# Optimization experiments

Measured on AMD Instinct MI355X. Metric: run time of the kernel, lower is better.

## Reference

```python
import jax, jax.numpy as jnp
import numpy as np

N = 4096      # nodes
F = 128       # input feature dim
HEADS = 8     # attention_num
U = 8         # units per head


def setup_inputs() -> dict:
    key = jax.random.key(0)
    k_a, k_h, k_w, k_al, k_ar = jax.random.split(key, 5)
    A = jax.random.randint(k_a, (N, N), 0, 2).astype(jnp.float32)   # dense 0/1 adjacency
    H = jax.random.normal(k_h, (N, F), dtype=jnp.float32)
    W = jax.random.normal(k_w, (HEADS, F, U), dtype=jnp.float32) * 0.1
    a_left = jax.random.normal(k_al, (HEADS, U), dtype=jnp.float32) * 0.1
    a_right = jax.random.normal(k_ar, (HEADS, U), dtype=jnp.float32) * 0.1
    return {"A": A, "H": H, "W": W, "a_left": a_left, "a_right": a_right}


def reference(A, H, W, a_left, a_right):
    # Per-head attention logits: E[h,i,j] = e_left[h,i] + e_right[h,j]
    e_l = jnp.einsum('nf,hfu,hu->hn', H, W, a_left)    # [HEADS, N]
    e_r = jnp.einsum('nf,hfu,hu->hn', H, W, a_right)   # [HEADS, N]
    E = e_l[:, :, None] + e_r[:, None, :]              # [HEADS, N, N]
    # Faithful to original: denominator uses exp(E * A) (zeros in A -> exp(0)=1)
    denom = jnp.sum(jnp.exp(E * A[None]), axis=-1, keepdims=True)   # [HEADS, N, 1]
    Alpha = jnp.exp(E) / denom * A[None]               # masked attention weights
    # Aggregate then project: elu(Alpha @ H @ W) per head
    out = jax.nn.elu(jnp.einsum('hij,jf,hfu->hiu', Alpha, H, W))    # [HEADS, N, U]
    # is_output_layer=False -> concat heads along feature dim: [N, HEADS*U]
    return jnp.transpose(out, (1, 0, 2)).reshape(H.shape[0], HEADS * U)
```

## Files before the change

kernel.cpp:

```cpp
#include <hip/hip_runtime.h>
#include <hip/hip_bf16.h>

#define NN 4096
#define FF 128
#define NC 80
#define HPAD 136

typedef __attribute__((ext_vector_type(4))) float float4v;
typedef __attribute__((ext_vector_type(4))) unsigned int uint4v;
typedef __attribute__((ext_vector_type(8))) short short8;
typedef __attribute__((ext_vector_type(8))) unsigned short ushort8;
typedef __attribute__((ext_vector_type(4))) unsigned short ushort4v;

static __device__ inline unsigned short bfb(float x) {
    __hip_bfloat16 b = __float2bfloat16(x);
    return *(unsigned short*)&b;
}
static __device__ inline float bff(unsigned short u) {
    __hip_bfloat16 b = *(__hip_bfloat16*)&u;
    return __bfloat162float(b);
}

__global__ __launch_bounds__(128) void gat_prep(const float* __restrict__ H,
                                                const float* __restrict__ W,
                                                const float* __restrict__ al,
                                                const float* __restrict__ ar,
                                                float* __restrict__ expEl,
                                                __hip_bfloat16* __restrict__ Bp)
{
    __shared__ unsigned short Hhi[32 * HPAD], Hlo[32 * HPAD];
    __shared__ unsigned short Whi[16 * NC * 8], Wlo[16 * NC * 8];
    const int t  = threadIdx.x;
    const int j0 = blockIdx.x * 32;

    {
        const int jr = t >> 2, f0 = (t & 3) * 32;
        const float* src = H + (size_t)(j0 + jr) * FF + f0;
        unsigned short* dh = Hhi + jr * HPAD + f0;
        unsigned short* dl = Hlo + jr * HPAD + f0;
        #pragma unroll
        for (int i = 0; i < 32; i += 4) {
            float4v x = *(const float4v*)(src + i);
            ushort4v hv, lv;
            #pragma unroll
            for (int c2 = 0; c2 < 4; ++c2) {
                unsigned short h = bfb(x[c2]);
                hv[c2] = h;
                lv[c2] = bfb(x[c2] - bff(h));
            }
            *(ushort4v*)(dh + i) = hv;
            *(ushort4v*)(dl + i) = lv;
        }
    }
    {
        const int hu = t & 63;
        const int fb = (t >> 6) * 64;
        const float* wsrc = W + (size_t)(hu >> 3) * (FF * 8) + (hu & 7);
        #pragma unroll
        for (int g8 = 0; g8 < 8; ++g8) {
            const int f0 = fb + g8 * 8;
            ushort8 hv, lv;
            #pragma unroll
            for (int i = 0; i < 8; ++i) {
                float x = wsrc[(size_t)(f0 + i) * 8];
                unsigned short h = bfb(x);
                hv[i] = h; lv[i] = bfb(x - bff(h));
            }
            const int g = (f0 >> 5) * 4 + ((f0 >> 3) & 3);
            *(ushort8*)&Whi[((size_t)g * NC + hu) * 8] = hv;
            *(ushort8*)&Wlo[((size_t)g * NC + hu) * 8] = lv;
        }
    }
    {
        const int h  = t >> 4;
        const int f0 = (t & 15) * 8;
        float arv[8], alv[8];
        #pragma unroll
        for (int u = 0; u < 8; ++u) { arv[u] = ar[h * 8 + u]; alv[u] = al[h * 8 + u]; }
        ushort8 rh, rl, lh, ll;
        #pragma unroll
        for (int i = 0; i < 8; ++i) {
            const float* wp = W + (size_t)h * (FF * 8) + (size_t)(f0 + i) * 8;
            float sr = 0.f, sl = 0.f;
            #pragma unroll
            for (int u = 0; u < 8; ++u) { float w = wp[u]; sr += w * arv[u]; sl += w * alv[u]; }
            unsigned short a = bfb(sr); rh[i] = a; rl[i] = bfb(sr - bff(a));
            unsigned short b = bfb(sl); lh[i] = b; ll[i] = bfb(sl - bff(b));
        }
        const int g = (f0 >> 5) * 4 + ((f0 >> 3) & 3);
        *(ushort8*)&Whi[((size_t)g * NC + 64 + h) * 8] = rh;
        *(ushort8*)&Wlo[((size_t)g * NC + 64 + h) * 8] = rl;
        *(ushort8*)&Whi[((size_t)g * NC + 72 + h) * 8] = lh;
        *(ushort8*)&Wlo[((size_t)g * NC + 72 + h) * 8] = ll;
    }
    __syncthreads();

    const int w = t >> 6, lane = t & 63;
    const int m16 = lane & 15, q = lane >> 4;

    float4v acc[5] = {};
    #pragma unroll
    for (int kt = 0; kt < 4; ++kt) {
        short8 ahi = *(const short8*)&Hhi[(w * 16 + m16) * HPAD + kt * 32 + q * 8];
        short8 alo = *(const short8*)&Hlo[(w * 16 + m16) * HPAD + kt * 32 + q * 8];
        #pragma unroll
        for (int nt = 0; nt < 5; ++nt) {
            short8 bhi = *(const short8*)&Whi[((size_t)(kt * 4 + q) * NC + nt * 16 + m16) * 8];
            short8 blo = *(const short8*)&Wlo[((size_t)(kt * 4 + q) * NC + nt * 16 + m16) * 8];
            acc[nt] = __builtin_amdgcn_mfma_f32_16x16x32_bf16(ahi, bhi, acc[nt], 0, 0, 0);
            acc[nt] = __builtin_amdgcn_mfma_f32_16x16x32_bf16(alo, bhi, acc[nt], 0, 0, 0);
            acc[nt] = __builtin_amdgcn_mfma_f32_16x16x32_bf16(ahi, blo, acc[nt], 0, 0, 0);
        }
    }

    const int jbase = j0 + w * 16 + q * 4;
    float ex[4];
    #pragma unroll
    for (int r = 0; r < 4; ++r) ex[r] = expf(acc[4][r]);
    if (m16 >= 8) {
        #pragma unroll
        for (int r = 0; r < 4; ++r)
            expEl[(m16 - 8) * NN + jbase + r] = ex[r];
    }
    #pragma unroll
    for (int r = 0; r < 4; ++r) {
        const int j = jbase + r;
        const size_t base = ((size_t)((j >> 5) * 4 + ((j >> 3) & 3)) * NC) * 8 + (j & 7);
        #pragma unroll
        for (int nt = 0; nt < 4; ++nt) {
            const int srcl = (lane & 48) | (nt * 2 + (m16 >> 3));
            const float er = __shfl(ex[r], srcl);
            Bp[base + (size_t)(nt * 16 + m16) * 8] = __float2bfloat16(er * acc[nt][r]);
        }
        const float v = (m16 < 8) ? ex[r] : (m16 == 8 ? 1.0f : 0.0f);
        Bp[base + (size_t)(64 + m16) * 8] = __float2bfloat16(v);
    }
}

__global__ __launch_bounds__(256) void gat_gemm(const float* __restrict__ A,
                                                const __hip_bfloat16* __restrict__ Bp,
                                                float* __restrict__ Cp,
                                                int ktiles)
{
    const int rb   = blockIdx.x;
    const int kc   = blockIdx.y;
    const int wave = threadIdx.x >> 6;
    const int lane = threadIdx.x & 63;
    const int m16  = lane & 15;
    const int q    = lane >> 4;
    const int row0 = rb * 64 + wave * 16;

    float4v acc[5] = {};

    const int k0 = kc * (ktiles * 32);
    const unsigned int* Au = (const unsigned int*)A;
    const short* Bs = (const short*)Bp;
    const unsigned int* arow = Au + (size_t)(row0 + m16) * NN + q * 8;

    uint4v a0 = *(const uint4v*)(arow + k0);
    uint4v a1 = *(const uint4v*)(arow + k0 + 4);

    for (int kt = 0; kt < ktiles; ++kt) {
        const int kk = k0 + kt * 32;
        short8 afrag;
        afrag[0] = (short)(a0[0] >> 16); afrag[1] = (short)(a0[1] >> 16);
        afrag[2] = (short)(a0[2] >> 16); afrag[3] = (short)(a0[3] >> 16);
        afrag[4] = (short)(a1[0] >> 16); afrag[5] = (short)(a1[1] >> 16);
        afrag[6] = (short)(a1[2] >> 16); afrag[7] = (short)(a1[3] >> 16);

        if (kt + 1 < ktiles) {
            a0 = *(const uint4v*)(arow + kk + 32);
            a1 = *(const uint4v*)(arow + kk + 36);
        }

        const int ktg = kk >> 5;
        const short8* bbase = (const short8*)(Bs + ((size_t)(ktg * 4 + q) * NC) * 8);
        #pragma unroll
        for (int nt = 0; nt < 5; ++nt) {
            short8 bfrag = bbase[nt * 16 + m16];
            acc[nt] = __builtin_amdgcn_mfma_f32_16x16x32_bf16(afrag, bfrag, acc[nt], 0, 0, 0);
        }
    }

    float* cbase = Cp + (size_t)kc * NN * NC;
    #pragma unroll
    for (int nt = 0; nt < 5; ++nt) {
        #pragma unroll
        for (int r = 0; r < 4; ++r) {
            const int row = row0 + q * 4 + r;
            const int col = nt * 16 + m16;
            cbase[(size_t)row * NC + col] = acc[nt][r];
        }
    }
}

__global__ __launch_bounds__(256) void gat_epilogue(const float* __restrict__ Cp,
                                                    const float* __restrict__ expEl,
                                                    float* __restrict__ out,
                                                    int KC)
{
    const int idx = blockIdx.x * 256 + threadIdx.x;
    const int i = idx >> 6;
    const int c = idx & 63;
    const int h = c >> 3;

    float T = 0.f, S = 0.f, dg = 0.f;
    for (int kc = 0; kc < KC; ++kc) {
        const float* row = Cp + ((size_t)kc * NN + i) * NC;
        T  += row[c];
        S  += row[64 + h];
        dg += row[72];
    }
    const float el = expEl[h * NN + i];
    const float denom = ((float)NN - dg) + el * S;
    const float x = el * T / denom;
    const float y = x > 0.f ? x : expf(x) - 1.f;
    out[idx] = y;
}

extern "C" void kernel_launch(void* const* d_in, const int* in_sizes, int n_in,
                              void* d_out, int out_size, void* d_ws, size_t ws_size,
                              hipStream_t stream) {
    const float* A  = (const float*)d_in[0];
    const float* H  = (const float*)d_in[1];
    const float* W  = (const float*)d_in[2];
    const float* al = (const float*)d_in[3];
    const float* ar = (const float*)d_in[4];
    float* out = (float*)d_out;

    float* expEl = (float*)d_ws;
    __hip_bfloat16* Bp = (__hip_bfloat16*)((char*)d_ws + 131072);
    float* Cp = (float*)((char*)d_ws + 131072 + 655360);

    const size_t fixed = 131072 + 655360;
    int KC = 8;
    while (KC > 1 && fixed + (size_t)KC * NN * NC * 4 > ws_size) KC >>= 1;
    const int ktiles = NN / (KC * 32);

    gat_prep<<<NN / 32, 128, 0, stream>>>(H, W, al, ar, expEl, Bp);
    gat_gemm<<<dim3(NN / 64, KC), 256, 0, stream>>>(A, Bp, Cp, ktiles);
    gat_epilogue<<<NN * 64 / 256, 256, 0, stream>>>(Cp, expEl, out, KC);
}
```

Baseline: 122.3 us.

## Fuse split-K reduction and epilogue into GEMM via last-block atomic counter

Removes the separate epilogue kernel launch. Each split-K GEMM block now bumps a per-row-block atomic counter, and the last block to finish reduces the partial sums for that row block and applies the normalization and ELU. The counters are zeroed in the prep kernel. This saves one launch and its dependency gap, at the cost of a threadfence, an atomic, and a serialized reduction tail run by only 64 blocks.

Result: slower. 237.7 us (+94.4%).

```diff
diff --git a/kernel.cpp b/kernel.cpp
--- a/kernel.cpp
+++ b/kernel.cpp
@@ -26,12 +26,15 @@
                                                 const float* __restrict__ al,
                                                 const float* __restrict__ ar,
                                                 float* __restrict__ expEl,
-                                                __hip_bfloat16* __restrict__ Bp)
+                                                __hip_bfloat16* __restrict__ Bp,
+                                                int* __restrict__ counters)
 {
     __shared__ unsigned short Hhi[32 * HPAD], Hlo[32 * HPAD];
     __shared__ unsigned short Whi[16 * NC * 8], Wlo[16 * NC * 8];
     const int t  = threadIdx.x;
     const int j0 = blockIdx.x * 32;
+
+    if (blockIdx.x == 0 && t < 64) counters[t] = 0;
 
     {
         const int jr = t >> 2, f0 = (t & 3) * 32;
@@ -140,7 +143,10 @@
 __global__ __launch_bounds__(256) void gat_gemm(const float* __restrict__ A,
                                                 const __hip_bfloat16* __restrict__ Bp,
                                                 float* __restrict__ Cp,
-                                                int ktiles)
+                                                int* __restrict__ counters,
+                                                const float* __restrict__ expEl,
+                                                float* __restrict__ out,
+                                                int ktiles, int KC)
 {
     const int rb   = blockIdx.x;
     const int kc   = blockIdx.y;
@@ -192,30 +198,33 @@
             cbase[(size_t)row * NC + col] = acc[nt][r];
         }
     }
-}
-
-__global__ __launch_bounds__(256) void gat_epilogue(const float* __restrict__ Cp,
-                                                    const float* __restrict__ expEl,
-                                                    float* __restrict__ out,
-                                                    int KC)
-{
-    const int idx = blockIdx.x * 256 + threadIdx.x;
-    const int i = idx >> 6;
-    const int c = idx & 63;
-    const int h = c >> 3;
-
-    float T = 0.f, S = 0.f, dg = 0.f;
-    for (int kc = 0; kc < KC; ++kc) {
-        const float* row = Cp + ((size_t)kc * NN + i) * NC;
-        T  += row[c];
-        S  += row[64 + h];
-        dg += row[72];
-    }
-    const float el = expEl[h * NN + i];
-    const float denom = ((float)NN - dg) + el * S;
-    const float x = el * T / denom;
-    const float y = x > 0.f ? x : expf(x) - 1.f;
-    out[idx] = y;
+
+    __threadfence();
+    __syncthreads();
+    __shared__ int sOld;
+    if (threadIdx.x == 0)
+        sOld = __hip_atomic_fetch_add(&counters[rb], 1, __ATOMIC_ACQ_REL,
+                                      __HIP_MEMORY_SCOPE_AGENT);
+    __syncthreads();
+    if (sOld != KC - 1) return;
+    __threadfence();
+
+    for (int p = threadIdx.x; p < 64 * 64; p += 256) {
+        const int i = rb * 64 + (p >> 6);
+        const int c = p & 63;
+        const int h = c >> 3;
+        float T = 0.f, S = 0.f, dg = 0.f;
+        for (int k = 0; k < KC; ++k) {
+            const float* row = Cp + ((size_t)k * NN + i) * NC;
+            T  += __hip_atomic_load(&row[c],      __ATOMIC_RELAXED, __HIP_MEMORY_SCOPE_AGENT);
+            S  += __hip_atomic_load(&row[64 + h], __ATOMIC_RELAXED, __HIP_MEMORY_SCOPE_AGENT);
+            dg += __hip_atomic_load(&row[72],     __ATOMIC_RELAXED, __HIP_MEMORY_SCOPE_AGENT);
+        }
+        const float el = expEl[h * NN + i];
+        const float denom = ((float)NN - dg) + el * S;
+        const float x = el * T / denom;
+        out[(size_t)i * 64 + c] = x > 0.f ? x : expf(x) - 1.f;
+    }
 }
 
 extern "C" void kernel_launch(void* const* d_in, const int* in_sizes, int n_in,
@@ -230,14 +239,14 @@
 
     float* expEl = (float*)d_ws;
     __hip_bfloat16* Bp = (__hip_bfloat16*)((char*)d_ws + 131072);
-    float* Cp = (float*)((char*)d_ws + 131072 + 655360);
-
-    const size_t fixed = 131072 + 655360;
+    int* counters = (int*)((char*)d_ws + 131072 + 655360);
+    float* Cp = (float*)((char*)d_ws + 131072 + 655360 + 1024);
+
+    const size_t fixed = 131072 + 655360 + 1024;
     int KC = 8;
     while (KC > 1 && fixed + (size_t)KC * NN * NC * 4 > ws_size) KC >>= 1;
     const int ktiles = NN / (KC * 32);
 
-    gat_prep<<<NN / 32, 128, 0, stream>>>(H, W, al, ar, expEl, Bp);
-    gat_gemm<<<dim3(NN / 64, KC), 256, 0, stream>>>(A, Bp, Cp, ktiles);
-    gat_epilogue<<<NN * 64 / 256, 256, 0, stream>>>(Cp, expEl, out, KC);
-}
+    gat_prep<<<NN / 32, 128, 0, stream>>>(H, W, al, ar, expEl, Bp, counters);
+    gat_gemm<<<dim3(NN / 64, KC), 256, 0, stream>>>(A, Bp, Cp, counters, expEl, out, ktiles, KC);
+}
```

## Fuse split-K reduction and epilogue into GEMM via intra-block LDS reduction

Applied to the files above, without the earlier changes.

The GEMM now launches 256 blocks of 512 threads, one per 16-row strip. Each of the eight waves covers a 512-wide K slice, and the partial tiles are reduced through shared memory inside the block. The normalization and ELU epilogue then run in the same kernel. This removes the global split-K partial buffer round-trip and the separate epilogue launch. In exchange, each block has more waves and uses LDS, and the K split is fixed at 8, which may change occupancy and A-row reuse across waves.

New measurement: 116.0 us (median of 2 runs). 1.05x faster.

```diff
diff --git a/kernel.cpp b/kernel.cpp
--- a/kernel.cpp
+++ b/kernel.cpp
@@ -5,6 +5,7 @@
 #define FF 128
 #define NC 80
 #define HPAD 136
+#define LSTR 84
 
 typedef __attribute__((ext_vector_type(4))) float float4v;
 typedef __attribute__((ext_vector_type(4))) unsigned int uint4v;
@@ -137,22 +138,22 @@
     }
 }
 
-__global__ __launch_bounds__(256) void gat_gemm(const float* __restrict__ A,
+__global__ __launch_bounds__(512) void gat_gemm(const float* __restrict__ A,
                                                 const __hip_bfloat16* __restrict__ Bp,
-                                                float* __restrict__ Cp,
-                                                int ktiles)
+                                                const float* __restrict__ expEl,
+                                                float* __restrict__ out)
 {
+    __shared__ float Ls[8 * 16 * LSTR];
     const int rb   = blockIdx.x;
-    const int kc   = blockIdx.y;
     const int wave = threadIdx.x >> 6;
     const int lane = threadIdx.x & 63;
     const int m16  = lane & 15;
     const int q    = lane >> 4;
-    const int row0 = rb * 64 + wave * 16;
+    const int row0 = rb * 16;
 
     float4v acc[5] = {};
 
-    const int k0 = kc * (ktiles * 32);
+    const int k0 = wave * 512;
     const unsigned int* Au = (const unsigned int*)A;
     const short* Bs = (const short*)Bp;
     const unsigned int* arow = Au + (size_t)(row0 + m16) * NN + q * 8;
@@ -160,7 +161,8 @@
     uint4v a0 = *(const uint4v*)(arow + k0);
     uint4v a1 = *(const uint4v*)(arow + k0 + 4);
 
-    for (int kt = 0; kt < ktiles; ++kt) {
+    #pragma unroll 4
+    for (int kt = 0; kt < 16; ++kt) {
         const int kk = k0 + kt * 32;
         short8 afrag;
         afrag[0] = (short)(a0[0] >> 16); afrag[1] = (short)(a0[1] >> 16);
@@ -168,7 +170,7 @@
         afrag[4] = (short)(a1[0] >> 16); afrag[5] = (short)(a1[1] >> 16);
         afrag[6] = (short)(a1[2] >> 16); afrag[7] = (short)(a1[3] >> 16);
 
-        if (kt + 1 < ktiles) {
+        if (kt + 1 < 16) {
             a0 = *(const uint4v*)(arow + kk + 32);
             a1 = *(const uint4v*)(arow + kk + 36);
         }
@@ -182,40 +184,33 @@
         }
     }
 
-    float* cbase = Cp + (size_t)kc * NN * NC;
+    float* Lw = Ls + wave * (16 * LSTR);
     #pragma unroll
     for (int nt = 0; nt < 5; ++nt) {
         #pragma unroll
-        for (int r = 0; r < 4; ++r) {
-            const int row = row0 + q * 4 + r;
-            const int col = nt * 16 + m16;
-            cbase[(size_t)row * NC + col] = acc[nt][r];
-        }
-    }
-}
-
-__global__ __launch_bounds__(256) void gat_epilogue(const float* __restrict__ Cp,
-                                                    const float* __restrict__ expEl,
-                                                    float* __restrict__ out,
-                                                    int KC)
-{
-    const int idx = blockIdx.x * 256 + threadIdx.x;
-    const int i = idx >> 6;
-    const int c = idx & 63;
-    const int h = c >> 3;
-
-    float T = 0.f, S = 0.f, dg = 0.f;
-    for (int kc = 0; kc < KC; ++kc) {
-        const float* row = Cp + ((size_t)kc * NN + i) * NC;
-        T  += row[c];
-        S  += row[64 + h];
-        dg += row[72];
-    }
-    const float el = expEl[h * NN + i];
-    const float denom = ((float)NN - dg) + el * S;
-    const float x = el * T / denom;
-    const float y = x > 0.f ? x : expf(x) - 1.f;
-    out[idx] = y;
+        for (int r = 0; r < 4; ++r)
+            Lw[(q * 4 + r) * LSTR + nt * 16 + m16] = acc[nt][r];
+    }
+    __syncthreads();
+
+    #pragma unroll
+    for (int p = threadIdx.x; p < 1024; p += 512) {
+        const int il = p >> 6;
+        const int c  = p & 63;
+        const int h  = c >> 3;
+        float T = 0.f, S = 0.f, dg = 0.f;
+        #pragma unroll
+        for (int w = 0; w < 8; ++w) {
+            const float* rowp = Ls + w * (16 * LSTR) + il * LSTR;
+            T  += rowp[c];
+            S  += rowp[64 + h];
+            dg += rowp[72];
+        }
+        const float el = expEl[h * NN + row0 + il];
+        const float denom = ((float)NN - dg) + el * S;
+        const float x = el * T / denom;
+        out[(size_t)(row0 + il) * 64 + c] = x > 0.f ? x : expf(x) - 1.f;
+    }
 }
 
 extern "C" void kernel_launch(void* const* d_in, const int* in_sizes, int n_in,
@@ -230,14 +225,7 @@
 
     float* expEl = (float*)d_ws;
     __hip_bfloat16* Bp = (__hip_bfloat16*)((char*)d_ws + 131072);
-    float* Cp = (float*)((char*)d_ws + 131072 + 655360);
-
-    const size_t fixed = 131072 + 655360;
-    int KC = 8;
-    while (KC > 1 && fixed + (size_t)KC * NN * NC * 4 > ws_size) KC >>= 1;
-    const int ktiles = NN / (KC * 32);
 
     gat_prep<<<NN / 32, 128, 0, stream>>>(H, W, al, ar, expEl, Bp);
-    gat_gemm<<<dim3(NN / 64, KC), 256, 0, stream>>>(A, Bp, Cp, ktiles);
-    gat_epilogue<<<NN * 64 / 256, 256, 0, stream>>>(Cp, expEl, out, KC);
-}
+    gat_gemm<<<NN / 16, 512, 0, stream>>>(A, Bp, expEl, out);
+}
```
